# Optimization experiments

Measured on AMD Instinct MI355X. Metric: run time of the kernel, lower is better.

The kernel has to match this reference:

```python
import jax, jax.numpy as jnp
import numpy as np

# LIF neuron constants (standard mem_update)
THRESH = 0.5
LENS = 0.5
DECAY = 0.25
EPS = 1e-5
NUM_HEADS = 8

@jax.custom_vjp
def act_fun(mem):
    return (mem > THRESH).astype(mem.dtype)

def _act_fwd(mem):
    return act_fun(mem), mem

def _act_bwd(mem, g):
    surrogate = (jnp.abs(mem - THRESH) < LENS).astype(g.dtype)
    return (g * surrogate,)

act_fun.defvjp(_act_fwd, _act_bwd)

def mem_update(x):
    # x: (T, ...) -> binary spikes (T, ...) via recurrent LIF dynamics
    def step(carry, xt):
        mem_old, spike = carry
        # spike is detached in the reset gate (torch .detach())
        mem = mem_old * DECAY * (1.0 - jax.lax.stop_gradient(spike)) + xt
        s = act_fun(mem)
        return (mem, s), s
    init = (jnp.zeros_like(x[0]), jnp.zeros_like(x[0]))
    _, out = jax.lax.scan(step, init, x)
    return out

def bn(x, gamma, beta, mean, var):
    # inference-mode BatchNorm1d over channel dim of (T,B,C,L)
    inv = gamma / jnp.sqrt(var + EPS)
    return x * inv[None, None, :, None] + (beta - mean * inv)[None, None, :, None]

def setup_inputs() -> dict:
    key = jax.random.key(0)
    ks = jax.random.split(key, 11)
    T, B, C, L = 4, 2, 384, 1024
    s = 1.0 / np.sqrt(C)
    return {
        "x": jax.random.normal(ks[0], (T, B, C, L), jnp.float32),
        "W_w": jax.random.normal(ks[1], (2 * C, C), jnp.float32) * s,
        "bn1_gamma": jax.random.uniform(ks[2], (2 * C,), jnp.float32, 0.5, 1.5),
        "bn1_beta": jax.random.normal(ks[3], (2 * C,), jnp.float32) * 0.1,
        "bn1_mean": jax.random.normal(ks[4], (2 * C,), jnp.float32) * 0.1,
        "bn1_var": jax.random.uniform(ks[5], (2 * C,), jnp.float32, 0.5, 1.5),
        "proj_w": jax.random.normal(ks[6], (C, C), jnp.float32) * s,
        "bn2_gamma": jax.random.uniform(ks[7], (C,), jnp.float32, 0.5, 1.5),
        "bn2_beta": jax.random.normal(ks[8], (C,), jnp.float32) * 0.1,
        "bn2_mean": jax.random.normal(ks[9], (C,), jnp.float32) * 0.1,
        "bn2_var": jax.random.uniform(ks[10], (C,), jnp.float32, 0.5, 1.5),
    }

def reference(x, W_w, bn1_gamma, bn1_beta, bn1_mean, bn1_var, proj_w, bn2_gamma, bn2_beta, bn2_mean, bn2_var):
    T, B, C, L = x.shape
    H = NUM_HEADS
    d = C // H
    x_feat = x
    xs = mem_update(x)                                   # binary spikes (T,B,C,L)
    y = jnp.einsum('oc,tbcl->tbol', W_w, xs)             # 1x1 conv C->2C
    y = bn(y, bn1_gamma, bn1_beta, bn1_mean, bn1_var)
    y = y.reshape(T, B, H, 2 * d, L)
    y1, y2 = y[:, :, :, :d, :], y[:, :, :, d:, :]
    xr = xs.reshape(T, B, H, d, L)
    attn = jnp.einsum('tbhdl,tbhdm->tbhlm', y1, xr)      # (L,L) per head
    attn = mem_update(attn)                              # binary spikes
    out = jnp.einsum('tbhdl,tbhlm->tbhdm', y2, attn)
    out = out.reshape(T, B, C, L)
    out = mem_update(out)
    out = jnp.einsum('oc,tbcl->tbol', proj_w, out)       # Wproj 1x1
    out = bn(out, bn2_gamma, bn2_beta, bn2_mean, bn2_var)
    return out + x_feat
```

## Files before the change

kernel.cpp:

```cpp
#include <hip/hip_runtime.h>

#define T_  4
#define B_  2
#define C_  384
#define L_  1024
#define H_  8
#define C2_ 768

typedef __attribute__((ext_vector_type(8))) short short8;
typedef __attribute__((ext_vector_type(4))) float floatx4;
typedef __attribute__((ext_vector_type(16))) float floatx16;

__device__ __forceinline__ unsigned bf16_rne(float v) {
    unsigned u = __float_as_uint(v);
    u += 0x7FFFu + ((u >> 16) & 1u);
    return u >> 16;
}
__device__ __forceinline__ float bf16_to_f(unsigned h) { return __uint_as_float(h << 16); }
__device__ __forceinline__ void split3(float v, unsigned& hi, unsigned& mi, unsigned& lo) {
    hi = bf16_rne(v);
    float r1 = v - bf16_to_f(hi);
    mi = bf16_rne(r1);
    float r2 = r1 - bf16_to_f(mi);
    lo = bf16_rne(r2);
}

__global__ __launch_bounds__(256) void scan_and_split(
    const float* __restrict__ src, unsigned short* __restrict__ dstT,
    unsigned short* __restrict__ xsF,
    const float* __restrict__ Wa, int n4a,
    unsigned short* __restrict__ hia, unsigned short* __restrict__ mia,
    unsigned short* __restrict__ loa,
    const float* __restrict__ Wb, int n4b,
    unsigned short* __restrict__ hib, unsigned short* __restrict__ mib,
    unsigned short* __restrict__ lob) {
    __shared__ unsigned short tile[32][72];
    const int tid = threadIdx.x;
    if (blockIdx.x >= 384) {
        int i = (blockIdx.x - 384) * 256 + tid;
        const float* W; unsigned short *hi, *mi, *lo;
        if (i < n4a) { W = Wa; hi = hia; mi = mia; lo = loa; }
        else {
            i -= n4a;
            if (i >= n4b) return;
            W = Wb; hi = hib; mi = mib; lo = lob;
        }
        float4 v = ((const float4*)W)[i];
        float vv[4] = {v.x, v.y, v.z, v.w};
        union { unsigned short us[4]; uint2 u2; } h, m, l;
#pragma unroll
        for (int e = 0; e < 4; e++) {
            unsigned hh, mm, ll; split3(vv[e], hh, mm, ll);
            h.us[e] = (unsigned short)hh; m.us[e] = (unsigned short)mm; l.us[e] = (unsigned short)ll;
        }
        ((uint2*)hi)[i] = h.u2; ((uint2*)mi)[i] = m.u2; ((uint2*)lo)[i] = l.u2;
        return;
    }
    const int job = blockIdx.x;
    const int l0 = (job & 15) * 64;
    const int c0 = ((job >> 4) % 12) * 32;
    const int b  = job / 192;
    const int row = tid >> 3, seg = tid & 7;
    float mem[8], sp[8];
#pragma unroll
    for (int e = 0; e < 8; e++) { mem[e] = 0.f; sp[e] = 0.f; }
    const size_t base0 = ((size_t)(b*C_ + c0 + row))*L_ + l0 + seg*8;
    float4 nx0 = *(const float4*)(src + base0);
    float4 nx1 = *(const float4*)(src + base0 + 4);
    for (int t = 0; t < T_; t++) {
        float4 v0 = nx0, v1 = nx1;
        if (t < 3) {
            const size_t nb = ((size_t)(((t+1)*B_ + b)*C_ + c0 + row))*L_ + l0 + seg*8;
            nx0 = *(const float4*)(src + nb);
            nx1 = *(const float4*)(src + nb + 4);
        }
        float vv[8] = {v0.x,v0.y,v0.z,v0.w,v1.x,v1.y,v1.z,v1.w};
        unsigned bs[8];
#pragma unroll
        for (int e = 0; e < 8; e++) {
            mem[e] = mem[e]*0.25f*(1.f - sp[e]) + vv[e];
            bool sb = mem[e] > 0.5f;
            sp[e] = sb ? 1.f : 0.f;
            bs[e] = sb ? 0x3F80u : 0u;
        }
#pragma unroll
        for (int p2 = 0; p2 < 4; p2++)
            *(unsigned*)&tile[row][seg*8 + p2*2] = bs[p2*2] | (bs[p2*2+1] << 16);
        __syncthreads();
        {
            const int lr = tid >> 2, cs = tid & 3;
            unsigned wv[4];
#pragma unroll
            for (int p = 0; p < 4; p++) {
                unsigned e0 = tile[cs*8 + p*2][lr];
                unsigned e1 = tile[cs*8 + p*2 + 1][lr];
                wv[p] = e0 | (e1 << 16);
            }
            uint4 o; o.x = wv[0]; o.y = wv[1]; o.z = wv[2]; o.w = wv[3];
            const int cc = c0 + cs*8;
            *(uint4*)(dstT + ((size_t)(t*B_ + b)*L_ + l0 + lr)*C_ + cc) = o;
            const int hh = cc / 48, kc = (cc % 48) >> 3;
            *(uint4*)(xsF + ((((size_t)(t*B_ + b)*H_ + hh)*6 + kc)*L_ + l0 + lr)*8) = o;
        }
        __syncthreads();
    }
}

__global__ __launch_bounds__(256) void scan_transpose2(
    const float* __restrict__ srcA, const float* __restrict__ srcB,
    unsigned short* __restrict__ dstT) {
    __shared__ unsigned short tile[32][72];
    const int tid = threadIdx.x;
    const int job = blockIdx.x;
    const int l0 = (job & 15) * 64;
    const int c0 = ((job >> 4) % 12) * 32;
    const int b  = job / 192;
    const int row = tid >> 3, seg = tid & 7;
    float mem[8], sp[8];
#pragma unroll
    for (int e = 0; e < 8; e++) { mem[e] = 0.f; sp[e] = 0.f; }
    const size_t base0 = ((size_t)(b*C_ + c0 + row))*L_ + l0 + seg*8;
    float4 na0 = *(const float4*)(srcA + base0);
    float4 na1 = *(const float4*)(srcA + base0 + 4);
    float4 nb0 = *(const float4*)(srcB + base0);
    float4 nb1 = *(const float4*)(srcB + base0 + 4);
    for (int t = 0; t < T_; t++) {
        float4 a0 = na0, a1 = na1, b0 = nb0, b1 = nb1;
        if (t < 3) {
            const size_t nb = ((size_t)(((t+1)*B_ + b)*C_ + c0 + row))*L_ + l0 + seg*8;
            na0 = *(const float4*)(srcA + nb);
            na1 = *(const float4*)(srcA + nb + 4);
            nb0 = *(const float4*)(srcB + nb);
            nb1 = *(const float4*)(srcB + nb + 4);
        }
        float vv[8] = {a0.x+b0.x, a0.y+b0.y, a0.z+b0.z, a0.w+b0.w,
                       a1.x+b1.x, a1.y+b1.y, a1.z+b1.z, a1.w+b1.w};
        unsigned bs[8];
#pragma unroll
        for (int e = 0; e < 8; e++) {
            mem[e] = mem[e]*0.25f*(1.f - sp[e]) + vv[e];
            bool sb = mem[e] > 0.5f;
            sp[e] = sb ? 1.f : 0.f;
            bs[e] = sb ? 0x3F80u : 0u;
        }
#pragma unroll
        for (int p2 = 0; p2 < 4; p2++)
            *(unsigned*)&tile[row][seg*8 + p2*2] = bs[p2*2] | (bs[p2*2+1] << 16);
        __syncthreads();
        {
            const int lr = tid >> 2, cs = tid & 3;
            unsigned wv[4];
#pragma unroll
            for (int p = 0; p < 4; p++) {
                unsigned e0 = tile[cs*8 + p*2][lr];
                unsigned e1 = tile[cs*8 + p*2 + 1][lr];
                wv[p] = e0 | (e1 << 16);
            }
            uint4 o; o.x = wv[0]; o.y = wv[1]; o.z = wv[2]; o.w = wv[3];
            *(uint4*)(dstT + ((size_t)(t*B_ + b)*L_ + l0 + lr)*C_ + c0 + cs*8) = o;
        }
        __syncthreads();
    }
}

__global__ __launch_bounds__(256) void gemm1_mfma(
    const unsigned short* __restrict__ whi, const unsigned short* __restrict__ wmi,
    const unsigned short* __restrict__ wlo, const unsigned short* __restrict__ xsT,
    const float* __restrict__ g, const float* __restrict__ be,
    const float* __restrict__ mn, const float* __restrict__ vr,
    unsigned short* __restrict__ y1hi, unsigned short* __restrict__ y1mi,
    unsigned short* __restrict__ y1lo,
    unsigned short* __restrict__ y2hi, unsigned short* __restrict__ y2mi,
    unsigned short* __restrict__ y2lo) {
    __shared__ unsigned short smem[14080];
    const int tid = threadIdx.x;
    const int flat = blockIdx.x;
    const int tb = flat & 7;
    const int ii = flat >> 3;
    const int mt = ii >> 4, lt = ii & 15;
    const int l0 = lt * 64;
    const int w = tid >> 6, lane = tid & 63;
    const int q = lane >> 4, n15 = lane & 15;
    const int mw = (w & 1) * 48, lw = (w >> 1) * 32;

    floatx4 acc[3][2];
#pragma unroll
    for (int i = 0; i < 3; i++)
#pragma unroll
        for (int j = 0; j < 2; j++) acc[i][j] = (floatx4){0.f,0.f,0.f,0.f};

    for (int ck = 0; ck < C_; ck += 32) {
#pragma unroll
        for (int p = 0; p < 3; p++) {
            const unsigned short* wp = p == 0 ? whi : p == 1 ? wmi : wlo;
            unsigned short* ap = smem + p*3840;
            for (int s = tid; s < 384; s += 256) {
                int r = s >> 2, c = s & 3;
                *(uint4*)&ap[r*40 + c*8] = *(const uint4*)(wp + (size_t)(mt*96 + r)*C_ + ck + c*8);
            }
        }
        {
            int r = tid >> 2, c = tid & 3;
            *(uint4*)&smem[11520 + r*40 + c*8] =
                *(const uint4*)(xsT + ((size_t)tb*L_ + l0 + r)*C_ + ck + c*8);
        }
        __syncthreads();
        short8 bb[2];
#pragma unroll
        for (int in = 0; in < 2; in++)
            bb[in] = *(short8*)&smem[11520 + (lw + in*16 + n15)*40 + q*8];
#pragma unroll
        for (int im = 0; im < 3; im++) {
            short8 ah = *(short8*)&smem[       (mw + im*16 + n15)*40 + q*8];
            short8 am = *(short8*)&smem[3840 + (mw + im*16 + n15)*40 + q*8];
            short8 al = *(short8*)&smem[7680 + (mw + im*16 + n15)*40 + q*8];
#pragma unroll
            for (int in = 0; in < 2; in++) {
                acc[im][in] = __builtin_amdgcn_mfma_f32_16x16x32_bf16(ah, bb[in], acc[im][in], 0,0,0);
                acc[im][in] = __builtin_amdgcn_mfma_f32_16x16x32_bf16(am, bb[in], acc[im][in], 0,0,0);
                acc[im][in] = __builtin_amdgcn_mfma_f32_16x16x32_bf16(al, bb[in], acc[im][in], 0,0,0);
            }
        }
        __syncthreads();
    }

#pragma unroll
    for (int im = 0; im < 3; im++)
#pragma unroll
        for (int r = 0; r < 4; r++) {
            int o = mt*96 + mw + im*16 + q*4 + r;
            float inv = g[o] / sqrtf(vr[o] + 1e-5f);
            float sh = be[o] - mn[o]*inv;
#pragma unroll
            for (int in = 0; in < 2; in++)
                acc[im][in][r] = acc[im][in][r]*inv + sh;
        }
    const bool isY1 = ((w & 1) == 0);
#pragma unroll
    for (int p = 0; p < 3; p++) {
        if (isY1) {
#pragma unroll
            for (int im = 0; im < 3; im++)
#pragma unroll
                for (int in = 0; in < 2; in++) {
                    union { unsigned short us[4]; uint2 u2; } pk;
#pragma unroll
                    for (int r = 0; r < 4; r++) {
                        unsigned hh = bf16_rne(acc[im][in][r]);
                        pk.us[r] = (unsigned short)hh;
                        acc[im][in][r] -= bf16_to_f(hh);
                    }
                    *(uint2*)&smem[(lw + in*16 + n15)*56 + im*16 + q*4] = pk.u2;
                }
        } else {
#pragma unroll
            for (int im = 0; im < 3; im++)
#pragma unroll
                for (int in = 0; in < 2; in++)
#pragma unroll
                    for (int r = 0; r < 4; r++) {
                        unsigned hh = bf16_rne(acc[im][in][r]);
                        smem[3584 + (im*16 + q*4 + r)*72 + lw + in*16 + n15] = (unsigned short)hh;
                        acc[im][in][r] -= bf16_to_f(hh);
                    }
        }
        __syncthreads();
        unsigned short* y1p = p == 0 ? y1hi : p == 1 ? y1mi : y1lo;
        unsigned short* y2p = p == 0 ? y2hi : p == 1 ? y2mi : y2lo;
        for (int s = tid; s < 384; s += 256) {
            int c8 = s >> 6, r1 = s & 63;
            *(uint4*)(y1p + ((((size_t)tb*H_ + mt)*6 + c8)*L_ + l0 + r1)*8) =
                *(uint4*)&smem[r1*56 + c8*8];
        }
        for (int s = tid; s < 384; s += 256) {
            int cr = s >> 3, lq = s & 7;
            *(uint4*)(y2p + ((size_t)tb*C_ + mt*48 + cr)*L_ + l0 + lq*8) =
                *(uint4*)&smem[3584 + cr*72 + lq*8];
        }
        __syncthreads();
    }
}

__global__ __launch_bounds__(256, 4) void attn_spike_mfma(
    const unsigned short* __restrict__ y1hi, const unsigned short* __restrict__ y1mi,
    const unsigned short* __restrict__ y1lo, const unsigned short* __restrict__ xsF,
    unsigned* __restrict__ bits) {
    const int tid = threadIdx.x;
    const int flat = blockIdx.x;
    const int xcd = flat & 7;
    const int ii = flat >> 3;
    const int bh = xcd*2 + (ii >> 7);
    const int rr = ii & 127;
    const int b = bh >> 3, h = bh & 7;
    const int lbase = (rr >> 3) * 64;
    const int mbase = (rr & 7) * 128;
    const int w = tid >> 6, lane = tid & 63;
    const int l31 = lane & 31, half = lane >> 5;
    const int mrow = mbase + w*32 + l31;

    float mem[2][16];
#pragma unroll
    for (int il = 0; il < 2; il++)
#pragma unroll
        for (int r = 0; r < 16; r++) mem[il][r] = 0.f;

    for (int t = 0; t < T_; t++) {
        const int tb = t*B_ + b;
        const size_t fb = ((size_t)tb*H_ + h)*6*L_*8;
        const unsigned short* ya_hi = y1hi + fb;
        const unsigned short* ya_mi = y1mi + fb;
        const unsigned short* ya_lo = y1lo + fb;
        const unsigned short* xf    = xsF  + fb;

        short8 bb[3];
#pragma unroll
        for (int ks = 0; ks < 3; ks++)
            bb[ks] = *(const short8*)(xf + ((size_t)(ks*2 + half)*L_ + mrow)*8);

        floatx16 acc[2];
#pragma unroll
        for (int il = 0; il < 2; il++)
#pragma unroll
            for (int r = 0; r < 16; r++) acc[il][r] = 0.f;

#pragma unroll
        for (int ks = 0; ks < 3; ks++) {
#pragma unroll
            for (int il = 0; il < 2; il++) {
                const size_t aoff = ((size_t)(ks*2 + half)*L_ + lbase + il*32 + l31)*8;
                short8 ah = *(const short8*)(ya_hi + aoff);
                short8 am = *(const short8*)(ya_mi + aoff);
                short8 al = *(const short8*)(ya_lo + aoff);
                acc[il] = __builtin_amdgcn_mfma_f32_32x32x16_bf16(ah, bb[ks], acc[il], 0,0,0);
                acc[il] = __builtin_amdgcn_mfma_f32_32x32x16_bf16(am, bb[ks], acc[il], 0,0,0);
                acc[il] = __builtin_amdgcn_mfma_f32_32x32x16_bf16(al, bb[ks], acc[il], 0,0,0);
            }
        }

        unsigned wds[2];
#pragma unroll
        for (int il = 0; il < 2; il++) {
            unsigned word = 0;
#pragma unroll
            for (int r = 0; r < 16; r++) {
                float m = (mem[il][r] > 0.5f ? 0.f : mem[il][r]*0.25f) + acc[il][r];
                mem[il][r] = m;
                int lloc = (r & 3) + 8*(r >> 2) + 4*half;
                word |= (m > 0.5f) ? (1u << lloc) : 0u;
            }
            wds[il] = word;
        }
        unsigned f0 = wds[0] | __shfl_xor(wds[0], 32);
        unsigned f1 = wds[1] | __shfl_xor(wds[1], 32);
        if (half == 0) {
            uint2 o; o.x = f0; o.y = f1;
            ((uint2*)bits)[((size_t)(tb*H_ + h)*16 + (lbase >> 6))*1024 + mrow] = o;
        }
    }
}

__global__ __launch_bounds__(256) void attn_out_mfma(
    const unsigned short* __restrict__ y2hi, const unsigned short* __restrict__ y2mi,
    const unsigned short* __restrict__ y2lo,
    const unsigned* __restrict__ bits,
    float* __restrict__ outpre, float* __restrict__ outpre2) {
    __shared__ unsigned short A_hi[48][72], A_mi[48][72], A_lo[48][72];
    const int tid = threadIdx.x;
    const int flat = blockIdx.x;
    const int xcd = flat & 7;
    const int ii = flat >> 3;
    const int tbh = xcd*8 + (ii >> 4);
    const int mtile = (ii >> 1) & 7;
    const int ls = ii & 1;
    const int t = tbh >> 4, b = (tbh >> 3) & 1, h = tbh & 7;
    const int tb = t*B_ + b;
    const int w = tid >> 6, lane = tid & 63;
    const int q = lane >> 4, n15 = lane & 15;
    const int mb = mtile*128 + w*32;
    const int lt0 = ls * 512;

    floatx4 acc[3][2];
#pragma unroll
    for (int i = 0; i < 3; i++)
#pragma unroll
        for (int in = 0; in < 2; in++) acc[i][in] = (floatx4){0.f,0.f,0.f,0.f};

    const uint2* bvec = (const uint2*)bits;
    const size_t bbase = ((size_t)(tb*H_ + h)*16)*1024 + mb + n15;
    const size_t y2b = ((size_t)tb*C_ + h*48)*L_;

    const int r0 = tid >> 3, c0i = tid & 7;
    const int r1 = (tid + 256) >> 3, c1i = tid & 7;
    uint4 rh0, rm0, rl0, rh1, rm1, rl1;
    {
        size_t ro = y2b + (size_t)r0*L_ + lt0 + c0i*8;
        rh0 = *(const uint4*)(y2hi + ro); rm0 = *(const uint4*)(y2mi + ro); rl0 = *(const uint4*)(y2lo + ro);
        if (tid < 128) {
            size_t ro1 = y2b + (size_t)r1*L_ + lt0 + c1i*8;
            rh1 = *(const uint4*)(y2hi + ro1); rm1 = *(const uint4*)(y2mi + ro1); rl1 = *(const uint4*)(y2lo + ro1);
        }
    }

    for (int it = 0; it < 8; it++) {
        const int lt = lt0 + it*64;
        *(uint4*)&A_hi[r0][c0i*8] = rh0; *(uint4*)&A_mi[r0][c0i*8] = rm0; *(uint4*)&A_lo[r0][c0i*8] = rl0;
        if (tid < 128) {
            *(uint4*)&A_hi[r1][c1i*8] = rh1; *(uint4*)&A_mi[r1][c1i*8] = rm1; *(uint4*)&A_lo[r1][c1i*8] = rl1;
        }
        uint2 bw0 = bvec[bbase + (size_t)(lt >> 6)*1024];
        uint2 bw1 = bvec[bbase + (size_t)(lt >> 6)*1024 + 16];
        __syncthreads();
        if (it < 7) {
            size_t ro = y2b + (size_t)r0*L_ + (lt + 64) + c0i*8;
            rh0 = *(const uint4*)(y2hi + ro); rm0 = *(const uint4*)(y2mi + ro); rl0 = *(const uint4*)(y2lo + ro);
            if (tid < 128) {
                size_t ro1 = y2b + (size_t)r1*L_ + (lt + 64) + c1i*8;
                rh1 = *(const uint4*)(y2hi + ro1); rm1 = *(const uint4*)(y2mi + ro1); rl1 = *(const uint4*)(y2lo + ro1);
            }
        }
#pragma unroll
        for (int kc = 0; kc < 2; kc++) {
            unsigned word0 = kc ? bw0.y : bw0.x;
            unsigned word1 = kc ? bw1.y : bw1.x;
            unsigned byt0 = (word0 >> (q*8)) & 0xFFu;
            unsigned byt1 = (word1 >> (q*8)) & 0xFFu;
            union { unsigned u[4]; short8 v; } bu0, bu1;
#pragma unroll
            for (int p = 0; p < 4; p++) {
                bu0.u[p] = (((byt0 >> (2*p)) & 1u) ? 0x3F80u : 0u)
                         | (((byt0 >> (2*p+1)) & 1u) ? 0x3F800000u : 0u);
                bu1.u[p] = (((byt1 >> (2*p)) & 1u) ? 0x3F80u : 0u)
                         | (((byt1 >> (2*p+1)) & 1u) ? 0x3F800000u : 0u);
            }
            short8 bf0 = bu0.v, bf1 = bu1.v;
#pragma unroll
            for (int i = 0; i < 3; i++) {
                int ra = i*16 + n15;
                short8 ah = *(short8*)&A_hi[ra][kc*32 + q*8];
                short8 am = *(short8*)&A_mi[ra][kc*32 + q*8];
                short8 al = *(short8*)&A_lo[ra][kc*32 + q*8];
                acc[i][0] = __builtin_amdgcn_mfma_f32_16x16x32_bf16(ah, bf0, acc[i][0], 0,0,0);
                acc[i][0] = __builtin_amdgcn_mfma_f32_16x16x32_bf16(am, bf0, acc[i][0], 0,0,0);
                acc[i][0] = __builtin_amdgcn_mfma_f32_16x16x32_bf16(al, bf0, acc[i][0], 0,0,0);
                acc[i][1] = __builtin_amdgcn_mfma_f32_16x16x32_bf16(ah, bf1, acc[i][1], 0,0,0);
                acc[i][1] = __builtin_amdgcn_mfma_f32_16x16x32_bf16(am, bf1, acc[i][1], 0,0,0);
                acc[i][1] = __builtin_amdgcn_mfma_f32_16x16x32_bf16(al, bf1, acc[i][1], 0,0,0);
            }
        }
        __syncthreads();
    }
    float* outP = ls ? outpre2 : outpre;
#pragma unroll
    for (int i = 0; i < 3; i++)
#pragma unroll
        for (int r = 0; r < 4; r++) {
            int d = i*16 + q*4 + r;
#pragma unroll
            for (int in = 0; in < 2; in++)
                outP[((size_t)tb*C_ + h*48 + d)*L_ + mb + in*16 + n15] = acc[i][in][r];
        }
}

__global__ __launch_bounds__(256) void gemm2_mfma(
    const unsigned short* __restrict__ whi, const unsigned short* __restrict__ wmi,
    const unsigned short* __restrict__ wlo, const unsigned short* __restrict__ xT,
    const float* __restrict__ g, const float* __restrict__ be,
    const float* __restrict__ mn, const float* __restrict__ vr,
    const float* __restrict__ res, float* __restrict__ out) {
    __shared__ unsigned short A_hi[96][40], A_mi[96][40], A_lo[96][40];
    __shared__ unsigned short B_s[64][40];
    const int tid = threadIdx.x;
    const int tb = blockIdx.y;
    const int mt = blockIdx.x >> 4, lt = blockIdx.x & 15;
    const int l0 = lt * 64;
    const int w = tid >> 6, lane = tid & 63;
    const int q = lane >> 4, n15 = lane & 15;
    const int mw = (w & 1) * 48, lw = (w >> 1) * 32;

    floatx4 acc[3][2];
#pragma unroll
    for (int i = 0; i < 3; i++)
#pragma unroll
        for (int j = 0; j < 2; j++) acc[i][j] = (floatx4){0.f,0.f,0.f,0.f};

    for (int ck = 0; ck < C_; ck += 32) {
#pragma unroll
        for (int p = 0; p < 3; p++) {
            const unsigned short* wp = p == 0 ? whi : p == 1 ? wmi : wlo;
            unsigned short (*ap)[40] = p == 0 ? A_hi : p == 1 ? A_mi : A_lo;
            for (int s = tid; s < 384; s += 256) {
                int r = s >> 2, c = s & 3;
                *(uint4*)&ap[r][c*8] = *(const uint4*)(wp + (size_t)(mt*96 + r)*C_ + ck + c*8);
            }
        }
        {
            int r = tid >> 2, c4 = tid & 3;
            *(uint4*)&B_s[r][c4*8] = *(const uint4*)(xT + ((size_t)tb*L_ + l0 + r)*C_ + ck + c4*8);
        }
        __syncthreads();
        short8 bb[2];
#pragma unroll
        for (int in = 0; in < 2; in++)
            bb[in] = *(short8*)&B_s[lw + in*16 + n15][q*8];
#pragma unroll
        for (int im = 0; im < 3; im++) {
            short8 ah = *(short8*)&A_hi[mw + im*16 + n15][q*8];
            short8 am = *(short8*)&A_mi[mw + im*16 + n15][q*8];
            short8 al = *(short8*)&A_lo[mw + im*16 + n15][q*8];
#pragma unroll
            for (int in = 0; in < 2; in++) {
                acc[im][in] = __builtin_amdgcn_mfma_f32_16x16x32_bf16(ah, bb[in], acc[im][in], 0,0,0);
                acc[im][in] = __builtin_amdgcn_mfma_f32_16x16x32_bf16(am, bb[in], acc[im][in], 0,0,0);
                acc[im][in] = __builtin_amdgcn_mfma_f32_16x16x32_bf16(al, bb[in], acc[im][in], 0,0,0);
            }
        }
        __syncthreads();
    }
#pragma unroll
    for (int im = 0; im < 3; im++)
#pragma unroll
        for (int r = 0; r < 4; r++) {
            int o = mt*96 + mw + im*16 + q*4 + r;
            float inv = g[o] / sqrtf(vr[o] + 1e-5f);
            float sh = be[o] - mn[o]*inv;
#pragma unroll
            for (int in = 0; in < 2; in++) {
                int l = l0 + lw + in*16 + n15;
                size_t idx = ((size_t)tb*C_ + o)*L_ + l;
                out[idx] = acc[im][in][r]*inv + sh + res[idx];
            }
        }
}

extern "C" void kernel_launch(void* const* d_in, const int* in_sizes, int n_in,
                              void* d_out, int out_size, void* d_ws, size_t ws_size,
                              hipStream_t stream) {
    const float* x   = (const float*)d_in[0];
    const float* W_w = (const float*)d_in[1];
    const float* g1  = (const float*)d_in[2];
    const float* b1  = (const float*)d_in[3];
    const float* m1  = (const float*)d_in[4];
    const float* v1  = (const float*)d_in[5];
    const float* pw  = (const float*)d_in[6];
    const float* g2  = (const float*)d_in[7];
    const float* b2  = (const float*)d_in[8];
    const float* m2  = (const float*)d_in[9];
    const float* v2  = (const float*)d_in[10];

    float* ws = (float*)d_ws;
    unsigned short* xsT  = (unsigned short*)ws;
    unsigned short* y1hi = (unsigned short*)(ws + 1572864);
    unsigned short* y1mi = (unsigned short*)(ws + 3145728);
    unsigned short* y1lo = (unsigned short*)(ws + 4718592);
    unsigned short* y2hi = (unsigned short*)(ws + 6291456);
    unsigned short* y2mi = (unsigned short*)(ws + 7864320);
    unsigned short* y2lo = (unsigned short*)(ws + 9437184);
    unsigned*       bits = (unsigned*)(ws + 11010048);
    unsigned short* wspl[3]  = {(unsigned short*)(ws + 13107200),
                                (unsigned short*)(ws + 13254656),
                                (unsigned short*)(ws + 13402112)};
    unsigned short* pwspl[3] = {(unsigned short*)(ws + 13549568),
                                (unsigned short*)(ws + 13623296),
                                (unsigned short*)(ws + 13697024)};
    unsigned short* xsF  = (unsigned short*)(ws + 13770752);
    float*          outpre  = (float*)(ws + 1572864);
    float*          outpre2 = (float*)(ws + 14557184);
    unsigned short* outsT   = (unsigned short*)(ws + 4718592);
    float* out = (float*)d_out;

    scan_and_split<<<dim3(816), 256, 0, stream>>>(x, xsT, xsF,
                                                  W_w, C2_*C_/4, wspl[0], wspl[1], wspl[2],
                                                  pw,  C_*C_/4, pwspl[0], pwspl[1], pwspl[2]);
    gemm1_mfma<<<dim3(1024), 256, 0, stream>>>(wspl[0], wspl[1], wspl[2], xsT,
                                               g1, b1, m1, v1,
                                               y1hi, y1mi, y1lo, y2hi, y2mi, y2lo);
    attn_spike_mfma<<<dim3(2048), 256, 0, stream>>>(y1hi, y1mi, y1lo, xsF, bits);
    attn_out_mfma<<<dim3(1024), 256, 0, stream>>>(y2hi, y2mi, y2lo, bits, outpre, outpre2);
    scan_transpose2<<<dim3(384), 256, 0, stream>>>(outpre, outpre2, outsT);
    gemm2_mfma<<<dim3(64, 8), 256, 0, stream>>>(pwspl[0], pwspl[1], pwspl[2], outsT,
                                                g2, b2, m2, v2, x, out);
}
```

Measured before the change: 212.3 us.

## Prefetch next K-slice into registers in gemm1 and pad LDS rows

The gemm1 main loop now loads the next 32-wide K slice of the three weight splits and the spike tile into registers while the MFMAs for the current slice run, then stores them to shared memory at the start of the next iteration. This is meant to hide global load latency behind compute. The shared-memory row stride also changes from 40 to 44 shorts to alter bank mapping. In exchange it uses more registers and more LDS, and the stride of 44 makes the 16-byte LDS accesses only 8-byte aligned.

```diff
diff --git a/kernel.cpp b/kernel.cpp
--- a/kernel.cpp
+++ b/kernel.cpp
@@ -172,7 +172,7 @@
     unsigned short* __restrict__ y1lo,
     unsigned short* __restrict__ y2hi, unsigned short* __restrict__ y2mi,
     unsigned short* __restrict__ y2lo) {
-    __shared__ unsigned short smem[14080];
+    __shared__ unsigned short smem[15488];
     const int tid = threadIdx.x;
     const int flat = blockIdx.x;
     const int tb = flat & 7;
@@ -189,31 +189,50 @@
 #pragma unroll
         for (int j = 0; j < 2; j++) acc[i][j] = (floatx4){0.f,0.f,0.f,0.f};
 
+    const int ar0 = tid >> 2, ac = tid & 3;
+    const int ar1 = (tid + 256) >> 2;
+    const int br = tid >> 2, bc = tid & 3;
+    const size_t wrow0 = (size_t)(mt*96 + ar0)*C_;
+    const size_t wrow1 = (size_t)(mt*96 + ar1)*C_;
+    const size_t brow  = ((size_t)tb*L_ + l0 + br)*C_;
+
+    uint4 rA[3][2]; uint4 rB;
+#pragma unroll
+    for (int p = 0; p < 3; p++) {
+        const unsigned short* wp = p == 0 ? whi : p == 1 ? wmi : wlo;
+        rA[p][0] = *(const uint4*)(wp + wrow0 + ac*8);
+        if (tid < 128) rA[p][1] = *(const uint4*)(wp + wrow1 + ac*8);
+    }
+    rB = *(const uint4*)(xsT + brow + bc*8);
+
     for (int ck = 0; ck < C_; ck += 32) {
 #pragma unroll
         for (int p = 0; p < 3; p++) {
-            const unsigned short* wp = p == 0 ? whi : p == 1 ? wmi : wlo;
-            unsigned short* ap = smem + p*3840;
-            for (int s = tid; s < 384; s += 256) {
-                int r = s >> 2, c = s & 3;
-                *(uint4*)&ap[r*40 + c*8] = *(const uint4*)(wp + (size_t)(mt*96 + r)*C_ + ck + c*8);
-            }
-        }
-        {
-            int r = tid >> 2, c = tid & 3;
-            *(uint4*)&smem[11520 + r*40 + c*8] =
-                *(const uint4*)(xsT + ((size_t)tb*L_ + l0 + r)*C_ + ck + c*8);
-        }
-        __syncthreads();
+            unsigned short* ap = smem + p*4224;
+            *(uint4*)&ap[ar0*44 + ac*8] = rA[p][0];
+            if (tid < 128) *(uint4*)&ap[ar1*44 + ac*8] = rA[p][1];
+        }
+        *(uint4*)&smem[12672 + br*44 + bc*8] = rB;
+        __syncthreads();
+        if (ck + 32 < C_) {
+            const int nk = ck + 32;
+#pragma unroll
+            for (int p = 0; p < 3; p++) {
+                const unsigned short* wp = p == 0 ? whi : p == 1 ? wmi : wlo;
+                rA[p][0] = *(const uint4*)(wp + wrow0 + nk + ac*8);
+                if (tid < 128) rA[p][1] = *(const uint4*)(wp + wrow1 + nk + ac*8);
+            }
+            rB = *(const uint4*)(xsT + brow + nk + bc*8);
+        }
         short8 bb[2];
 #pragma unroll
         for (int in = 0; in < 2; in++)
-            bb[in] = *(short8*)&smem[11520 + (lw + in*16 + n15)*40 + q*8];
+            bb[in] = *(short8*)&smem[12672 + (lw + in*16 + n15)*44 + q*8];
 #pragma unroll
         for (int im = 0; im < 3; im++) {
-            short8 ah = *(short8*)&smem[       (mw + im*16 + n15)*40 + q*8];
-            short8 am = *(short8*)&smem[3840 + (mw + im*16 + n15)*40 + q*8];
-            short8 al = *(short8*)&smem[7680 + (mw + im*16 + n15)*40 + q*8];
+            short8 ah = *(short8*)&smem[       (mw + im*16 + n15)*44 + q*8];
+            short8 am = *(short8*)&smem[4224 + (mw + im*16 + n15)*44 + q*8];
+            short8 al = *(short8*)&smem[8448 + (mw + im*16 + n15)*44 + q*8];
 #pragma unroll
             for (int in = 0; in < 2; in++) {
                 acc[im][in] = __builtin_amdgcn_mfma_f32_16x16x32_bf16(ah, bb[in], acc[im][in], 0,0,0);
```

Result: slower. 251.5 us (+18.5%).
